# Optimization experiments

Hardware: AMD Instinct MI355X
Metric: run time of the kernel (lower is better)

The kernel has to match this reference:

```python
import jax, jax.numpy as jnp
import numpy as np

H = 1024
V = 50257
S = 2048


def setup_inputs() -> dict:
    key = jax.random.key(0)
    ks = jax.random.split(key, 20)
    sd = 1.0 / np.sqrt(H)
    inp = {
        "input": jax.random.randint(ks[0], (1,), 0, V, dtype=jnp.int64) if jax.config.jax_enable_x64 else jax.random.randint(ks[0], (1,), 0, V, dtype=jnp.int32),
        "hidden": jax.random.normal(ks[1], (1, 1, H), dtype=jnp.float32),
        "encoder_hiddens": jax.random.normal(ks[2], (S, H), dtype=jnp.float32),
        "emb": jax.random.normal(ks[3], (V, H), dtype=jnp.float32),
        "Ua_w": jax.random.normal(ks[4], (H, H), dtype=jnp.float32) * sd,
        "Ua_b": jax.random.normal(ks[5], (H,), dtype=jnp.float32) * sd,
        "Wa_w": jax.random.normal(ks[6], (H, H), dtype=jnp.float32) * sd,
        "Wa_b": jax.random.normal(ks[7], (H,), dtype=jnp.float32) * sd,
        "va": jax.random.normal(ks[8], (1, H), dtype=jnp.float32),
        "comb_w": jax.random.normal(ks[9], (H, 2 * H), dtype=jnp.float32) * sd,
        "comb_b": jax.random.normal(ks[10], (H,), dtype=jnp.float32) * sd,
        "gru_w_ih": jax.random.normal(ks[11], (3 * H, H), dtype=jnp.float32) * sd,
        "gru_w_hh": jax.random.normal(ks[12], (3 * H, H), dtype=jnp.float32) * sd,
        "gru_b_ih": jax.random.normal(ks[13], (3 * H,), dtype=jnp.float32) * sd,
        "gru_b_hh": jax.random.normal(ks[14], (3 * H,), dtype=jnp.float32) * sd,
        "out_w": jax.random.normal(ks[15], (V, 2 * H), dtype=jnp.float32) * sd,
        "out_b": jax.random.normal(ks[16], (V,), dtype=jnp.float32) * sd,
    }
    return inp


def reference(input, hidden, encoder_hiddens, emb, Ua_w, Ua_b, Wa_w, Wa_b, va,
              comb_w, comb_b, gru_w_ih, gru_w_hh, gru_b_ih, gru_b_hh, out_w, out_b):
    # embedded: [1,1,H]  (dropout is identity in eval / p handled at train time)
    embedded = emb[input].reshape(1, 1, H)
    enc = encoder_hiddens[:, None, :]  # [S,1,H]
    # Bahdanau scores: tanh(Ua(enc) + Wa(hidden)) -> [S,1,H]
    scores = jnp.tanh(enc @ Ua_w.T + Ua_b + hidden @ Wa_w.T + Wa_b)
    # torch.inner(va [1,H], scores [S,1,H]) -> [1,S,1]; softmax over S
    attn_weights = jax.nn.softmax(jnp.einsum('oh,sbh->osb', va, scores), axis=1)
    # context: sum_s attn[1,S,1] * enc[S,H] -> [1,H]
    context = jnp.sum(attn_weights * encoder_hiddens, axis=1)
    # combine + relu -> GRU input x: [1,H]
    x = jax.nn.relu(jnp.concatenate([embedded[0], context], axis=1) @ comb_w.T + comb_b)
    # single GRU cell step (PyTorch gate layout: r, z, n)
    h0 = hidden[0]  # [1,H]
    gi = x @ gru_w_ih.T + gru_b_ih
    gh = h0 @ gru_w_hh.T + gru_b_hh
    i_r, i_z, i_n = jnp.split(gi, 3, axis=1)
    h_r, h_z, h_n = jnp.split(gh, 3, axis=1)
    r = jax.nn.sigmoid(i_r + h_r)
    z = jax.nn.sigmoid(i_z + h_z)
    n = jnp.tanh(i_n + r * h_n)
    h_new = (1.0 - z) * n + z * h0  # [1,H]
    hidden_out = h_new[None]  # [1,1,H]
    cat_output = jnp.concatenate([context, h_new], axis=1)  # [1,2H]
    log_probs = jax.nn.log_softmax(cat_output @ out_w.T + out_b, axis=1)  # [1,V]
    return (log_probs, hidden_out, attn_weights)
```

## Files before the change

### kernel.cpp

```cpp
#include <hip/hip_runtime.h>
#include <math.h>

#define H 1024
#define V 50257
#define S 2048

typedef unsigned short u16;
typedef __attribute__((ext_vector_type(8))) short short8;
typedef __attribute__((ext_vector_type(4))) float floatx4;

__device__ __forceinline__ float b2f(u16 b) {
    union { unsigned int u; float f; } x; x.u = ((unsigned int)b) << 16; return x.f;
}
__device__ __forceinline__ u16 f2b(float f) {
    union { float f; unsigned int u; } x; x.f = f;
    unsigned int r = x.u + 0x7FFFu + ((x.u >> 16) & 1u);
    return (u16)(r >> 16);
}

__global__ void __launch_bounds__(256) matvec_kernel(
    const float* __restrict__ W,
    const float* __restrict__ xa, const int* __restrict__ xa_idx, int Ka,
    const float* __restrict__ xb, int Kb,
    const float* __restrict__ bias1,
    float* __restrict__ out, int rows, int relu_flag)
{
    int wave = threadIdx.x >> 6;
    int lane = threadIdx.x & 63;
    int r = blockIdx.x * 4 + wave;
    if (r >= rows) return;
    const float* Wr = W + (size_t)r * (Ka + Kb);
    if (xa_idx) xa += (size_t)(*xa_idx) * Ka;
    float dot = 0.f;
    for (int base = 0; base < Ka; base += 256) {
        int k = base + lane * 4;
        float4 w4 = *reinterpret_cast<const float4*>(Wr + k);
        float4 a4 = *reinterpret_cast<const float4*>(xa + k);
        dot += w4.x * a4.x + w4.y * a4.y + w4.z * a4.z + w4.w * a4.w;
    }
    for (int base = 0; base < Kb; base += 256) {
        int k = base + lane * 4;
        float4 w4 = *reinterpret_cast<const float4*>(Wr + Ka + k);
        float4 a4 = *reinterpret_cast<const float4*>(xb + k);
        dot += w4.x * a4.x + w4.y * a4.y + w4.z * a4.z + w4.w * a4.w;
    }
    #pragma unroll
    for (int off = 32; off; off >>= 1) dot += __shfl_down(dot, off);
    if (lane == 0) {
        float v = dot + bias1[r];
        if (relu_flag) v = fmaxf(v, 0.f);
        out[r] = v;
    }
}

__global__ void __launch_bounds__(256) prep_kernel(
    const float* __restrict__ Wa_w, const float* __restrict__ hidden,
    const float* __restrict__ Wa_b, const float* __restrict__ Ua_b,
    float* __restrict__ u_vec, float* __restrict__ ws_zero,
    const float* __restrict__ enc, const float* __restrict__ Ua,
    u16* __restrict__ enc_hi, u16* __restrict__ enc_lo,
    u16* __restrict__ Ua_hi, u16* __restrict__ Ua_lo)
{
    unsigned int zidx = blockIdx.x * 256 + threadIdx.x;
    if (zidx < 4097) ws_zero[zidx] = 0.f;

    if (blockIdx.x < 256) {
        int wave = threadIdx.x >> 6, lane = threadIdx.x & 63;
        int r = blockIdx.x * 4 + wave;
        const float* Wr = Wa_w + (size_t)r * H;
        float dot = 0.f;
        #pragma unroll
        for (int t = 0; t < 4; t++) {
            int k = t * 256 + lane * 4;
            float4 w4 = *reinterpret_cast<const float4*>(Wr + k);
            float4 a4 = *reinterpret_cast<const float4*>(hidden + k);
            dot += w4.x * a4.x + w4.y * a4.y + w4.z * a4.z + w4.w * a4.w;
        }
        #pragma unroll
        for (int off = 32; off; off >>= 1) dot += __shfl_down(dot, off);
        if (lane == 0) u_vec[r] = dot + Wa_b[r] + Ua_b[r];
        return;
    }
    int idx = (blockIdx.x - 256) * 1024 + threadIdx.x * 4;
    const float* src; u16 *dhi, *dlo; int off;
    if (idx < S * H) { src = enc; dhi = enc_hi; dlo = enc_lo; off = idx; }
    else             { src = Ua;  dhi = Ua_hi;  dlo = Ua_lo;  off = idx - S * H; }
    float4 a = *reinterpret_cast<const float4*>(src + off);
    float av[4] = {a.x, a.y, a.z, a.w};
    ushort4 hi4, lo4;
    u16 hv[4], lv[4];
    #pragma unroll
    for (int i = 0; i < 4; i++) {
        u16 h = f2b(av[i]);
        hv[i] = h;
        lv[i] = f2b(av[i] - b2f(h));
    }
    hi4.x = hv[0]; hi4.y = hv[1]; hi4.z = hv[2]; hi4.w = hv[3];
    lo4.x = lv[0]; lo4.y = lv[1]; lo4.z = lv[2]; lo4.w = lv[3];
    *reinterpret_cast<ushort4*>(dhi + off) = hi4;
    *reinterpret_cast<ushort4*>(dlo + off) = lo4;
}

__global__ void __launch_bounds__(256) attn_scores_kernel(
    const u16* __restrict__ enc_hi, const u16* __restrict__ enc_lo,
    const u16* __restrict__ Ua_hi, const u16* __restrict__ Ua_lo,
    const float* __restrict__ va, const float* __restrict__ u,
    float* __restrict__ attn_logits)
{
    int sgrp  = blockIdx.x & 15;
    int jtile = blockIdx.x >> 4;
    int wave = threadIdx.x >> 6;
    int lane = threadIdx.x & 63;
    int l15 = lane & 15, quad = lane >> 4;
    int s0 = sgrp * 128 + wave * 32, j0 = jtile * 64;

    floatx4 zero4 = {0.f, 0.f, 0.f, 0.f};
    floatx4 acc[2][4];
    #pragma unroll
    for (int ra = 0; ra < 2; ra++)
        #pragma unroll
        for (int cb = 0; cb < 4; cb++) acc[ra][cb] = zero4;

    size_t aoff = (size_t)(s0 + l15) * H + quad * 8;
    size_t boff = (size_t)(j0 + l15) * H + quad * 8;

    for (int k0 = 0; k0 < H; k0 += 32) {
        short8 ah0 = *reinterpret_cast<const short8*>(enc_hi + aoff + k0);
        short8 al0 = *reinterpret_cast<const short8*>(enc_lo + aoff + k0);
        short8 ah1 = *reinterpret_cast<const short8*>(enc_hi + aoff + 16 * H + k0);
        short8 al1 = *reinterpret_cast<const short8*>(enc_lo + aoff + 16 * H + k0);
        #pragma unroll
        for (int cb = 0; cb < 4; cb++) {
            size_t bo = boff + (size_t)cb * 16 * H + k0;
            short8 bh = *reinterpret_cast<const short8*>(Ua_hi + bo);
            short8 bl = *reinterpret_cast<const short8*>(Ua_lo + bo);
            acc[0][cb] = __builtin_amdgcn_mfma_f32_16x16x32_bf16(ah0, bh, acc[0][cb], 0, 0, 0);
            acc[0][cb] = __builtin_amdgcn_mfma_f32_16x16x32_bf16(ah0, bl, acc[0][cb], 0, 0, 0);
            acc[0][cb] = __builtin_amdgcn_mfma_f32_16x16x32_bf16(al0, bh, acc[0][cb], 0, 0, 0);
            acc[1][cb] = __builtin_amdgcn_mfma_f32_16x16x32_bf16(ah1, bh, acc[1][cb], 0, 0, 0);
            acc[1][cb] = __builtin_amdgcn_mfma_f32_16x16x32_bf16(ah1, bl, acc[1][cb], 0, 0, 0);
            acc[1][cb] = __builtin_amdgcn_mfma_f32_16x16x32_bf16(al1, bh, acc[1][cb], 0, 0, 0);
        }
    }

    #pragma unroll
    for (int ra = 0; ra < 2; ra++) {
        #pragma unroll
        for (int reg = 0; reg < 4; reg++) {
            float p = 0.f;
            #pragma unroll
            for (int cb = 0; cb < 4; cb++) {
                int jj = j0 + cb * 16 + l15;
                p += va[jj] * tanhf(acc[ra][cb][reg] + u[jj]);
            }
            p += __shfl_xor(p, 1); p += __shfl_xor(p, 2);
            p += __shfl_xor(p, 4); p += __shfl_xor(p, 8);
            if (l15 == 0)
                atomicAdd(&attn_logits[s0 + ra * 16 + quad * 4 + reg], p);
        }
    }
}

__global__ void __launch_bounds__(256) softmax_context_kernel(
    const float* __restrict__ logits, const float* __restrict__ enc,
    float* __restrict__ ctx, float* __restrict__ attn_out)
{
    __shared__ float red[256];
    __shared__ float sw[16];
    int tid = threadIdx.x;
    float vals[8];
    float m = -1e30f;
    #pragma unroll
    for (int i = 0; i < 8; i++) { vals[i] = logits[tid + 256 * i]; m = fmaxf(m, vals[i]); }
    red[tid] = m; __syncthreads();
    for (int s = 128; s > 0; s >>= 1) {
        if (tid < s) red[tid] = fmaxf(red[tid], red[tid + s]);
        __syncthreads();
    }
    float gmax = red[0]; __syncthreads();
    float sum = 0.f;
    #pragma unroll
    for (int i = 0; i < 8; i++) { vals[i] = expf(vals[i] - gmax); sum += vals[i]; }
    red[tid] = sum; __syncthreads();
    for (int s = 128; s > 0; s >>= 1) {
        if (tid < s) red[tid] += red[tid + s];
        __syncthreads();
    }
    float inv = 1.f / red[0];

    if (blockIdx.x == 0) {
        #pragma unroll
        for (int i = 0; i < 8; i++) attn_out[tid + 256 * i] = vals[i] * inv;
    }

    int sbase = blockIdx.x * 16;
    if (tid < 16) sw[tid] = expf(logits[sbase + tid] - gmax) * inv;
    __syncthreads();

    int h = tid * 4;
    float p0 = 0.f, p1 = 0.f, p2 = 0.f, p3 = 0.f;
    #pragma unroll
    for (int i = 0; i < 16; i++) {
        float w = sw[i];
        float4 e = *reinterpret_cast<const float4*>(enc + (size_t)(sbase + i) * H + h);
        p0 = fmaf(w, e.x, p0); p1 = fmaf(w, e.y, p1);
        p2 = fmaf(w, e.z, p2); p3 = fmaf(w, e.w, p3);
    }
    atomicAdd(&ctx[h + 0], p0); atomicAdd(&ctx[h + 1], p1);
    atomicAdd(&ctx[h + 2], p2); atomicAdd(&ctx[h + 3], p3);
}

__global__ void __launch_bounds__(256) gru_fused_kernel(
    const float* __restrict__ w_ih, const float* __restrict__ w_hh,
    const float* __restrict__ x, const float* __restrict__ h0,
    const float* __restrict__ b_ih, const float* __restrict__ b_hh,
    float* __restrict__ cat_hnew, float* __restrict__ out_hidden)
{
    int wave = threadIdx.x >> 6, lane = threadIdx.x & 63;
    int j = blockIdx.x * 4 + wave;
    float d[6] = {0.f, 0.f, 0.f, 0.f, 0.f, 0.f};
    #pragma unroll
    for (int t = 0; t < 4; t++) {
        int k = t * 256 + lane * 4;
        float4 xv = *reinterpret_cast<const float4*>(x + k);
        float4 hv = *reinterpret_cast<const float4*>(h0 + k);
        #pragma unroll
        for (int g = 0; g < 3; g++) {
            float4 wi = *reinterpret_cast<const float4*>(w_ih + (size_t)(g * H + j) * H + k);
            float4 wh = *reinterpret_cast<const float4*>(w_hh + (size_t)(g * H + j) * H + k);
            d[g]     += wi.x * xv.x + wi.y * xv.y + wi.z * xv.z + wi.w * xv.w;
            d[3 + g] += wh.x * hv.x + wh.y * hv.y + wh.z * hv.z + wh.w * hv.w;
        }
    }
    #pragma unroll
    for (int off = 32; off; off >>= 1)
        #pragma unroll
        for (int g = 0; g < 6; g++) d[g] += __shfl_down(d[g], off);
    if (lane == 0) {
        float i_r = d[0] + b_ih[j];
        float i_z = d[1] + b_ih[H + j];
        float i_n = d[2] + b_ih[2 * H + j];
        float h_r = d[3] + b_hh[j];
        float h_z = d[4] + b_hh[H + j];
        float h_n = d[5] + b_hh[2 * H + j];
        float r = 1.f / (1.f + expf(-(i_r + h_r)));
        float z = 1.f / (1.f + expf(-(i_z + h_z)));
        float n = tanhf(i_n + r * h_n);
        float hn = (1.f - z) * n + z * h0[j];
        cat_hnew[j] = hn;
        out_hidden[j] = hn;
    }
}

__global__ void __launch_bounds__(256) out_matvec_kernel(
    const float* __restrict__ Wout, const float* __restrict__ bout,
    const float* __restrict__ cat, float* __restrict__ logits,
    float* __restrict__ separtial)
{
    __shared__ float cs[2 * H];
    __shared__ float wred[4];
    for (int i = threadIdx.x; i < 2 * H; i += 256) cs[i] = cat[i];
    __syncthreads();
    int wave = threadIdx.x >> 6, lane = threadIdx.x & 63;
    float lsum = 0.f;
    for (int v = blockIdx.x * 4 + wave; v < V; v += gridDim.x * 4) {
        const float* Wr = Wout + (size_t)v * (2 * H);
        float dot = 0.f;
        #pragma unroll
        for (int t = 0; t < 8; t++) {
            int k = t * 256 + lane * 4;
            float4 w4 = *reinterpret_cast<const float4*>(Wr + k);
            dot += w4.x * cs[k] + w4.y * cs[k + 1] + w4.z * cs[k + 2] + w4.w * cs[k + 3];
        }
        #pragma unroll
        for (int off = 32; off; off >>= 1) dot += __shfl_down(dot, off);
        if (lane == 0) {
            dot += bout[v];
            logits[v] = dot;
            lsum += expf(dot);
        }
    }
    if (lane == 0) wred[wave] = lsum;
    __syncthreads();
    if (threadIdx.x == 0)
        separtial[blockIdx.x] = wred[0] + wred[1] + wred[2] + wred[3];
}

__global__ void __launch_bounds__(256) logsoftmax_kernel(
    float* __restrict__ logits, const float* __restrict__ separtial)
{
    __shared__ float red[256];
    int tid = threadIdx.x;
    float s = 0.f;
    #pragma unroll
    for (int i = 0; i < 8; i++) s += separtial[tid + 256 * i];
    red[tid] = s; __syncthreads();
    for (int st = 128; st > 0; st >>= 1) {
        if (tid < st) red[tid] += red[tid + st];
        __syncthreads();
    }
    float lz = logf(red[0]);
    int v = blockIdx.x * 256 + tid;
    if (v < V) logits[v] -= lz;
}

extern "C" void kernel_launch(void* const* d_in, const int* in_sizes, int n_in,
                              void* d_out, int out_size, void* d_ws, size_t ws_size,
                              hipStream_t stream)
{
    const int*   token  = (const int*)d_in[0];
    const float* hidden = (const float*)d_in[1];
    const float* enc    = (const float*)d_in[2];
    const float* emb    = (const float*)d_in[3];
    const float* Ua_w   = (const float*)d_in[4];
    const float* Ua_b   = (const float*)d_in[5];
    const float* Wa_w   = (const float*)d_in[6];
    const float* Wa_b   = (const float*)d_in[7];
    const float* va     = (const float*)d_in[8];
    const float* comb_w = (const float*)d_in[9];
    const float* comb_b = (const float*)d_in[10];
    const float* w_ih   = (const float*)d_in[11];
    const float* w_hh   = (const float*)d_in[12];
    const float* b_ih   = (const float*)d_in[13];
    const float* b_hh   = (const float*)d_in[14];
    const float* out_w  = (const float*)d_in[15];
    const float* out_b  = (const float*)d_in[16];
    float* out = (float*)d_out;

    float* ws          = (float*)d_ws;
    float* attn_logits = ws + 0;
    float* cat         = ws + 2048;
    float* u_vec       = ws + 4608;
    float* x_vec       = ws + 5632;
    float* separtial   = ws + 6656;

    char* wsb   = (char*)d_ws;
    u16* enc_hi = (u16*)(wsb + 65536);
    u16* enc_lo = (u16*)(wsb + 65536 + 4u * 1024 * 1024);
    u16* Ua_hi  = (u16*)(wsb + 65536 + 8u * 1024 * 1024);
    u16* Ua_lo  = (u16*)(wsb + 65536 + 10u * 1024 * 1024);

    prep_kernel<<<3328, 256, 0, stream>>>(Wa_w, hidden, Wa_b, Ua_b, u_vec, ws,
                                          enc, Ua_w, enc_hi, enc_lo, Ua_hi, Ua_lo);
    attn_scores_kernel<<<256, 256, 0, stream>>>(enc_hi, enc_lo, Ua_hi, Ua_lo,
                                                va, u_vec, attn_logits);
    softmax_context_kernel<<<128, 256, 0, stream>>>(attn_logits, enc, cat,
                                                    out + V + H);
    matvec_kernel<<<256, 256, 0, stream>>>(comb_w, emb, token, H, cat, H,
                                           comb_b, x_vec, H, 1);
    gru_fused_kernel<<<256, 256, 0, stream>>>(w_ih, w_hh, x_vec, hidden,
                                              b_ih, b_hh, cat + H, out + V);
    out_matvec_kernel<<<2048, 256, 0, stream>>>(out_w, out_b, cat, out, separtial);
    logsoftmax_kernel<<<(V + 255) / 256, 256, 0, stream>>>(out, separtial);
}
```

Measured before the change: 751.2 us.

## Fuse attention, softmax-context, combine and GRU into one persistent kernel with grid barriers

Merges the attention-score MFMA, softmax+context, combine matvec and GRU input matvec into a single 256-block kernel separated by atomic spin grid barriers, removing three kernel launches and their gaps. The hidden-state GRU matvec (w_hh·h) is moved into the prep kernel as extra blocks since it depends only on inputs. The context reduction now uses 256 blocks of 8 rows instead of 128 of 16. This relies on all blocks being co-resident for the barrier to avoid deadlock, and adds spin-wait overhead.

Result: slower. 807.0 us (+7.4%).

```diff
diff --git a/kernel.cpp b/kernel.cpp
--- a/kernel.cpp
+++ b/kernel.cpp
@@ -4,6 +4,7 @@
 #define H 1024
 #define V 50257
 #define S 2048
+#define NBLK 256
 
 typedef unsigned short u16;
 typedef __attribute__((ext_vector_type(8))) short short8;
@@ -18,39 +19,17 @@
     return (u16)(r >> 16);
 }
 
-__global__ void __launch_bounds__(256) matvec_kernel(
-    const float* __restrict__ W,
-    const float* __restrict__ xa, const int* __restrict__ xa_idx, int Ka,
-    const float* __restrict__ xb, int Kb,
-    const float* __restrict__ bias1,
-    float* __restrict__ out, int rows, int relu_flag)
-{
-    int wave = threadIdx.x >> 6;
-    int lane = threadIdx.x & 63;
-    int r = blockIdx.x * 4 + wave;
-    if (r >= rows) return;
-    const float* Wr = W + (size_t)r * (Ka + Kb);
-    if (xa_idx) xa += (size_t)(*xa_idx) * Ka;
-    float dot = 0.f;
-    for (int base = 0; base < Ka; base += 256) {
-        int k = base + lane * 4;
-        float4 w4 = *reinterpret_cast<const float4*>(Wr + k);
-        float4 a4 = *reinterpret_cast<const float4*>(xa + k);
-        dot += w4.x * a4.x + w4.y * a4.y + w4.z * a4.z + w4.w * a4.w;
-    }
-    for (int base = 0; base < Kb; base += 256) {
-        int k = base + lane * 4;
-        float4 w4 = *reinterpret_cast<const float4*>(Wr + Ka + k);
-        float4 a4 = *reinterpret_cast<const float4*>(xb + k);
-        dot += w4.x * a4.x + w4.y * a4.y + w4.z * a4.z + w4.w * a4.w;
-    }
-    #pragma unroll
-    for (int off = 32; off; off >>= 1) dot += __shfl_down(dot, off);
-    if (lane == 0) {
-        float v = dot + bias1[r];
-        if (relu_flag) v = fmaxf(v, 0.f);
-        out[r] = v;
-    }
+__device__ __forceinline__ void grid_barrier(int* cnt) {
+    __syncthreads();
+    if (threadIdx.x == 0) {
+        __threadfence();
+        __hip_atomic_fetch_add(cnt, 1, __ATOMIC_ACQ_REL, __HIP_MEMORY_SCOPE_AGENT);
+        while (__hip_atomic_load(cnt, __ATOMIC_ACQUIRE, __HIP_MEMORY_SCOPE_AGENT) < NBLK) {
+            __builtin_amdgcn_s_sleep(1);
+        }
+        __threadfence();
+    }
+    __syncthreads();
 }
 
 __global__ void __launch_bounds__(256) prep_kernel(
@@ -59,10 +38,11 @@
     float* __restrict__ u_vec, float* __restrict__ ws_zero,
     const float* __restrict__ enc, const float* __restrict__ Ua,
     u16* __restrict__ enc_hi, u16* __restrict__ enc_lo,
-    u16* __restrict__ Ua_hi, u16* __restrict__ Ua_lo)
+    u16* __restrict__ Ua_hi, u16* __restrict__ Ua_lo,
+    const float* __restrict__ w_hh, float* __restrict__ gh)
 {
     unsigned int zidx = blockIdx.x * 256 + threadIdx.x;
-    if (zidx < 4097) ws_zero[zidx] = 0.f;
+    if (zidx < 4104) ws_zero[zidx] = 0.f;
 
     if (blockIdx.x < 256) {
         int wave = threadIdx.x >> 6, lane = threadIdx.x & 63;
@@ -81,174 +61,233 @@
         if (lane == 0) u_vec[r] = dot + Wa_b[r] + Ua_b[r];
         return;
     }
-    int idx = (blockIdx.x - 256) * 1024 + threadIdx.x * 4;
-    const float* src; u16 *dhi, *dlo; int off;
-    if (idx < S * H) { src = enc; dhi = enc_hi; dlo = enc_lo; off = idx; }
-    else             { src = Ua;  dhi = Ua_hi;  dlo = Ua_lo;  off = idx - S * H; }
-    float4 a = *reinterpret_cast<const float4*>(src + off);
-    float av[4] = {a.x, a.y, a.z, a.w};
-    ushort4 hi4, lo4;
-    u16 hv[4], lv[4];
-    #pragma unroll
-    for (int i = 0; i < 4; i++) {
-        u16 h = f2b(av[i]);
-        hv[i] = h;
-        lv[i] = f2b(av[i] - b2f(h));
-    }
-    hi4.x = hv[0]; hi4.y = hv[1]; hi4.z = hv[2]; hi4.w = hv[3];
-    lo4.x = lv[0]; lo4.y = lv[1]; lo4.z = lv[2]; lo4.w = lv[3];
-    *reinterpret_cast<ushort4*>(dhi + off) = hi4;
-    *reinterpret_cast<ushort4*>(dlo + off) = lo4;
-}
-
-__global__ void __launch_bounds__(256) attn_scores_kernel(
+    if (blockIdx.x < 3328) {
+        int idx = (blockIdx.x - 256) * 1024 + threadIdx.x * 4;
+        const float* src; u16 *dhi, *dlo; int off;
+        if (idx < S * H) { src = enc; dhi = enc_hi; dlo = enc_lo; off = idx; }
+        else             { src = Ua;  dhi = Ua_hi;  dlo = Ua_lo;  off = idx - S * H; }
+        float4 a = *reinterpret_cast<const float4*>(src + off);
+        float av[4] = {a.x, a.y, a.z, a.w};
+        ushort4 hi4, lo4;
+        u16 hv[4], lv[4];
+        #pragma unroll
+        for (int i = 0; i < 4; i++) {
+            u16 h = f2b(av[i]);
+            hv[i] = h;
+            lv[i] = f2b(av[i] - b2f(h));
+        }
+        hi4.x = hv[0]; hi4.y = hv[1]; hi4.z = hv[2]; hi4.w = hv[3];
+        lo4.x = lv[0]; lo4.y = lv[1]; lo4.z = lv[2]; lo4.w = lv[3];
+        *reinterpret_cast<ushort4*>(dhi + off) = hi4;
+        *reinterpret_cast<ushort4*>(dlo + off) = lo4;
+        return;
+    }
+    {
+        int wave = threadIdx.x >> 6, lane = threadIdx.x & 63;
+        int j = (blockIdx.x - 3328) * 4 + wave;
+        float d0 = 0.f, d1 = 0.f, d2 = 0.f;
+        #pragma unroll
+        for (int t = 0; t < 4; t++) {
+            int k = t * 256 + lane * 4;
+            float4 hv = *reinterpret_cast<const float4*>(hidden + k);
+            float4 w0 = *reinterpret_cast<const float4*>(w_hh + (size_t)(0 * H + j) * H + k);
+            float4 w1 = *reinterpret_cast<const float4*>(w_hh + (size_t)(1 * H + j) * H + k);
+            float4 w2 = *reinterpret_cast<const float4*>(w_hh + (size_t)(2 * H + j) * H + k);
+            d0 += w0.x * hv.x + w0.y * hv.y + w0.z * hv.z + w0.w * hv.w;
+            d1 += w1.x * hv.x + w1.y * hv.y + w1.z * hv.z + w1.w * hv.w;
+            d2 += w2.x * hv.x + w2.y * hv.y + w2.z * hv.z + w2.w * hv.w;
+        }
+        #pragma unroll
+        for (int off = 32; off; off >>= 1) {
+            d0 += __shfl_down(d0, off);
+            d1 += __shfl_down(d1, off);
+            d2 += __shfl_down(d2, off);
+        }
+        if (lane == 0) { gh[j] = d0; gh[H + j] = d1; gh[2 * H + j] = d2; }
+    }
+}
+
+__global__ void __launch_bounds__(256) mega_kernel(
     const u16* __restrict__ enc_hi, const u16* __restrict__ enc_lo,
     const u16* __restrict__ Ua_hi, const u16* __restrict__ Ua_lo,
     const float* __restrict__ va, const float* __restrict__ u,
-    float* __restrict__ attn_logits)
-{
-    int sgrp  = blockIdx.x & 15;
-    int jtile = blockIdx.x >> 4;
-    int wave = threadIdx.x >> 6;
-    int lane = threadIdx.x & 63;
-    int l15 = lane & 15, quad = lane >> 4;
-    int s0 = sgrp * 128 + wave * 32, j0 = jtile * 64;
-
-    floatx4 zero4 = {0.f, 0.f, 0.f, 0.f};
-    floatx4 acc[2][4];
-    #pragma unroll
-    for (int ra = 0; ra < 2; ra++)
-        #pragma unroll
-        for (int cb = 0; cb < 4; cb++) acc[ra][cb] = zero4;
-
-    size_t aoff = (size_t)(s0 + l15) * H + quad * 8;
-    size_t boff = (size_t)(j0 + l15) * H + quad * 8;
-
-    for (int k0 = 0; k0 < H; k0 += 32) {
-        short8 ah0 = *reinterpret_cast<const short8*>(enc_hi + aoff + k0);
-        short8 al0 = *reinterpret_cast<const short8*>(enc_lo + aoff + k0);
-        short8 ah1 = *reinterpret_cast<const short8*>(enc_hi + aoff + 16 * H + k0);
-        short8 al1 = *reinterpret_cast<const short8*>(enc_lo + aoff + 16 * H + k0);
-        #pragma unroll
-        for (int cb = 0; cb < 4; cb++) {
-            size_t bo = boff + (size_t)cb * 16 * H + k0;
-            short8 bh = *reinterpret_cast<const short8*>(Ua_hi + bo);
-            short8 bl = *reinterpret_cast<const short8*>(Ua_lo + bo);
-            acc[0][cb] = __builtin_amdgcn_mfma_f32_16x16x32_bf16(ah0, bh, acc[0][cb], 0, 0, 0);
-            acc[0][cb] = __builtin_amdgcn_mfma_f32_16x16x32_bf16(ah0, bl, acc[0][cb], 0, 0, 0);
-            acc[0][cb] = __builtin_amdgcn_mfma_f32_16x16x32_bf16(al0, bh, acc[0][cb], 0, 0, 0);
-            acc[1][cb] = __builtin_amdgcn_mfma_f32_16x16x32_bf16(ah1, bh, acc[1][cb], 0, 0, 0);
-            acc[1][cb] = __builtin_amdgcn_mfma_f32_16x16x32_bf16(ah1, bl, acc[1][cb], 0, 0, 0);
-            acc[1][cb] = __builtin_amdgcn_mfma_f32_16x16x32_bf16(al1, bh, acc[1][cb], 0, 0, 0);
-        }
-    }
-
-    #pragma unroll
-    for (int ra = 0; ra < 2; ra++) {
-        #pragma unroll
-        for (int reg = 0; reg < 4; reg++) {
-            float p = 0.f;
+    float* __restrict__ attn_logits,
+    const float* __restrict__ enc, float* __restrict__ cat,
+    float* __restrict__ attn_out,
+    const float* __restrict__ comb_w, const float* __restrict__ comb_b,
+    const float* __restrict__ emb, const int* __restrict__ token,
+    float* __restrict__ x_vec,
+    const float* __restrict__ w_ih, const float* __restrict__ b_ih,
+    const float* __restrict__ b_hh, const float* __restrict__ gh,
+    const float* __restrict__ hidden, float* __restrict__ out_hidden,
+    int* __restrict__ bars)
+{
+    __shared__ float red[256];
+    __shared__ float sw[8];
+    int tid  = threadIdx.x;
+    int wave = tid >> 6;
+    int lane = tid & 63;
+
+    {
+        int sgrp  = blockIdx.x & 15;
+        int jtile = blockIdx.x >> 4;
+        int l15 = lane & 15, quad = lane >> 4;
+        int s0 = sgrp * 128 + wave * 32, j0 = jtile * 64;
+
+        floatx4 zero4 = {0.f, 0.f, 0.f, 0.f};
+        floatx4 acc[2][4];
+        #pragma unroll
+        for (int ra = 0; ra < 2; ra++)
+            #pragma unroll
+            for (int cb = 0; cb < 4; cb++) acc[ra][cb] = zero4;
+
+        size_t aoff = (size_t)(s0 + l15) * H + quad * 8;
+        size_t boff = (size_t)(j0 + l15) * H + quad * 8;
+
+        for (int k0 = 0; k0 < H; k0 += 32) {
+            short8 ah0 = *reinterpret_cast<const short8*>(enc_hi + aoff + k0);
+            short8 al0 = *reinterpret_cast<const short8*>(enc_lo + aoff + k0);
+            short8 ah1 = *reinterpret_cast<const short8*>(enc_hi + aoff + 16 * H + k0);
+            short8 al1 = *reinterpret_cast<const short8*>(enc_lo + aoff + 16 * H + k0);
             #pragma unroll
             for (int cb = 0; cb < 4; cb++) {
-                int jj = j0 + cb * 16 + l15;
-                p += va[jj] * tanhf(acc[ra][cb][reg] + u[jj]);
+                size_t bo = boff + (size_t)cb * 16 * H + k0;
+                short8 bh = *reinterpret_cast<const short8*>(Ua_hi + bo);
+                short8 bl = *reinterpret_cast<const short8*>(Ua_lo + bo);
+                acc[0][cb] = __builtin_amdgcn_mfma_f32_16x16x32_bf16(ah0, bh, acc[0][cb], 0, 0, 0);
+                acc[0][cb] = __builtin_amdgcn_mfma_f32_16x16x32_bf16(ah0, bl, acc[0][cb], 0, 0, 0);
+                acc[0][cb] = __builtin_amdgcn_mfma_f32_16x16x32_bf16(al0, bh, acc[0][cb], 0, 0, 0);
+                acc[1][cb] = __builtin_amdgcn_mfma_f32_16x16x32_bf16(ah1, bh, acc[1][cb], 0, 0, 0);
+                acc[1][cb] = __builtin_amdgcn_mfma_f32_16x16x32_bf16(ah1, bl, acc[1][cb], 0, 0, 0);
+                acc[1][cb] = __builtin_amdgcn_mfma_f32_16x16x32_bf16(al1, bh, acc[1][cb], 0, 0, 0);
             }
-            p += __shfl_xor(p, 1); p += __shfl_xor(p, 2);
-            p += __shfl_xor(p, 4); p += __shfl_xor(p, 8);
-            if (l15 == 0)
-                atomicAdd(&attn_logits[s0 + ra * 16 + quad * 4 + reg], p);
-        }
-    }
-}
-
-__global__ void __launch_bounds__(256) softmax_context_kernel(
-    const float* __restrict__ logits, const float* __restrict__ enc,
-    float* __restrict__ ctx, float* __restrict__ attn_out)
-{
-    __shared__ float red[256];
-    __shared__ float sw[16];
-    int tid = threadIdx.x;
-    float vals[8];
-    float m = -1e30f;
-    #pragma unroll
-    for (int i = 0; i < 8; i++) { vals[i] = logits[tid + 256 * i]; m = fmaxf(m, vals[i]); }
-    red[tid] = m; __syncthreads();
-    for (int s = 128; s > 0; s >>= 1) {
-        if (tid < s) red[tid] = fmaxf(red[tid], red[tid + s]);
+        }
+
+        #pragma unroll
+        for (int ra = 0; ra < 2; ra++) {
+            #pragma unroll
+            for (int reg = 0; reg < 4; reg++) {
+                float p = 0.f;
+                #pragma unroll
+                for (int cb = 0; cb < 4; cb++) {
+                    int jj = j0 + cb * 16 + l15;
+                    p += va[jj] * tanhf(acc[ra][cb][reg] + u[jj]);
+                }
+                p += __shfl_xor(p, 1); p += __shfl_xor(p, 2);
+                p += __shfl_xor(p, 4); p += __shfl_xor(p, 8);
+                if (l15 == 0)
+                    atomicAdd(&attn_logits[s0 + ra * 16 + quad * 4 + reg], p);
+            }
+        }
+    }
+
+    grid_barrier(bars + 0);
+
+    {
+        float vals[8];
+        float m = -1e30f;
+        #pragma unroll
+        for (int i = 0; i < 8; i++) { vals[i] = attn_logits[tid + 256 * i]; m = fmaxf(m, vals[i]); }
+        red[tid] = m; __syncthreads();
+        for (int s = 128; s > 0; s >>= 1) {
+            if (tid < s) red[tid] = fmaxf(red[tid], red[tid + s]);
+            __syncthreads();
+        }
+        float gmax = red[0]; __syncthreads();
+        float sum = 0.f;
+        #pragma unroll
+        for (int i = 0; i < 8; i++) { vals[i] = expf(vals[i] - gmax); sum += vals[i]; }
+        red[tid] = sum; __syncthreads();
+        for (int s = 128; s > 0; s >>= 1) {
+            if (tid < s) red[tid] += red[tid + s];
+            __syncthreads();
+        }
+        float inv = 1.f / red[0];
+
+        if (blockIdx.x == 0) {
+            #pragma unroll
+            for (int i = 0; i < 8; i++) attn_out[tid + 256 * i] = vals[i] * inv;
+        }
+
+        int sbase = blockIdx.x * 8;
+        if (tid < 8) sw[tid] = expf(attn_logits[sbase + tid] - gmax) * inv;
         __syncthreads();
-    }
-    float gmax = red[0]; __syncthreads();
-    float sum = 0.f;
-    #pragma unroll
-    for (int i = 0; i < 8; i++) { vals[i] = expf(vals[i] - gmax); sum += vals[i]; }
-    red[tid] = sum; __syncthreads();
-    for (int s = 128; s > 0; s >>= 1) {
-        if (tid < s) red[tid] += red[tid + s];
-        __syncthreads();
-    }
-    float inv = 1.f / red[0];
-
-    if (blockIdx.x == 0) {
-        #pragma unroll
-        for (int i = 0; i < 8; i++) attn_out[tid + 256 * i] = vals[i] * inv;
-    }
-
-    int sbase = blockIdx.x * 16;
-    if (tid < 16) sw[tid] = expf(logits[sbase + tid] - gmax) * inv;
-    __syncthreads();
-
-    int h = tid * 4;
-    float p0 = 0.f, p1 = 0.f, p2 = 0.f, p3 = 0.f;
-    #pragma unroll
-    for (int i = 0; i < 16; i++) {
-        float w = sw[i];
-        float4 e = *reinterpret_cast<const float4*>(enc + (size_t)(sbase + i) * H + h);
-        p0 = fmaf(w, e.x, p0); p1 = fmaf(w, e.y, p1);
-        p2 = fmaf(w, e.z, p2); p3 = fmaf(w, e.w, p3);
-    }
-    atomicAdd(&ctx[h + 0], p0); atomicAdd(&ctx[h + 1], p1);
-    atomicAdd(&ctx[h + 2], p2); atomicAdd(&ctx[h + 3], p3);
-}
-
-__global__ void __launch_bounds__(256) gru_fused_kernel(
-    const float* __restrict__ w_ih, const float* __restrict__ w_hh,
-    const float* __restrict__ x, const float* __restrict__ h0,
-    const float* __restrict__ b_ih, const float* __restrict__ b_hh,
-    float* __restrict__ cat_hnew, float* __restrict__ out_hidden)
-{
-    int wave = threadIdx.x >> 6, lane = threadIdx.x & 63;
-    int j = blockIdx.x * 4 + wave;
-    float d[6] = {0.f, 0.f, 0.f, 0.f, 0.f, 0.f};
-    #pragma unroll
-    for (int t = 0; t < 4; t++) {
-        int k = t * 256 + lane * 4;
-        float4 xv = *reinterpret_cast<const float4*>(x + k);
-        float4 hv = *reinterpret_cast<const float4*>(h0 + k);
-        #pragma unroll
-        for (int g = 0; g < 3; g++) {
-            float4 wi = *reinterpret_cast<const float4*>(w_ih + (size_t)(g * H + j) * H + k);
-            float4 wh = *reinterpret_cast<const float4*>(w_hh + (size_t)(g * H + j) * H + k);
-            d[g]     += wi.x * xv.x + wi.y * xv.y + wi.z * xv.z + wi.w * xv.w;
-            d[3 + g] += wh.x * hv.x + wh.y * hv.y + wh.z * hv.z + wh.w * hv.w;
-        }
-    }
-    #pragma unroll
-    for (int off = 32; off; off >>= 1)
-        #pragma unroll
-        for (int g = 0; g < 6; g++) d[g] += __shfl_down(d[g], off);
-    if (lane == 0) {
-        float i_r = d[0] + b_ih[j];
-        float i_z = d[1] + b_ih[H + j];
-        float i_n = d[2] + b_ih[2 * H + j];
-        float h_r = d[3] + b_hh[j];
-        float h_z = d[4] + b_hh[H + j];
-        float h_n = d[5] + b_hh[2 * H + j];
-        float r = 1.f / (1.f + expf(-(i_r + h_r)));
-        float z = 1.f / (1.f + expf(-(i_z + h_z)));
-        float n = tanhf(i_n + r * h_n);
-        float hn = (1.f - z) * n + z * h0[j];
-        cat_hnew[j] = hn;
-        out_hidden[j] = hn;
+
+        int h = tid * 4;
+        float p0 = 0.f, p1 = 0.f, p2 = 0.f, p3 = 0.f;
+        #pragma unroll
+        for (int i = 0; i < 8; i++) {
+            float w = sw[i];
+            float4 e = *reinterpret_cast<const float4*>(enc + (size_t)(sbase + i) * H + h);
+            p0 = fmaf(w, e.x, p0); p1 = fmaf(w, e.y, p1);
+            p2 = fmaf(w, e.z, p2); p3 = fmaf(w, e.w, p3);
+        }
+        atomicAdd(&cat[h + 0], p0); atomicAdd(&cat[h + 1], p1);
+        atomicAdd(&cat[h + 2], p2); atomicAdd(&cat[h + 3], p3);
+    }
+
+    grid_barrier(bars + 1);
+
+    {
+        int r = blockIdx.x * 4 + wave;
+        const float* Wr = comb_w + (size_t)r * (2 * H);
+        const float* erow = emb + (size_t)(*token) * H;
+        float dot = 0.f;
+        #pragma unroll
+        for (int t = 0; t < 4; t++) {
+            int k = t * 256 + lane * 4;
+            float4 w4 = *reinterpret_cast<const float4*>(Wr + k);
+            float4 a4 = *reinterpret_cast<const float4*>(erow + k);
+            dot += w4.x * a4.x + w4.y * a4.y + w4.z * a4.z + w4.w * a4.w;
+        }
+        #pragma unroll
+        for (int t = 0; t < 4; t++) {
+            int k = t * 256 + lane * 4;
+            float4 w4 = *reinterpret_cast<const float4*>(Wr + H + k);
+            float4 a4 = *reinterpret_cast<const float4*>(cat + k);
+            dot += w4.x * a4.x + w4.y * a4.y + w4.z * a4.z + w4.w * a4.w;
+        }
+        #pragma unroll
+        for (int off = 32; off; off >>= 1) dot += __shfl_down(dot, off);
+        if (lane == 0) x_vec[r] = fmaxf(dot + comb_b[r], 0.f);
+    }
+
+    grid_barrier(bars + 2);
+
+    {
+        int j = blockIdx.x * 4 + wave;
+        float d0 = 0.f, d1 = 0.f, d2 = 0.f;
+        #pragma unroll
+        for (int t = 0; t < 4; t++) {
+            int k = t * 256 + lane * 4;
+            float4 xv = *reinterpret_cast<const float4*>(x_vec + k);
+            float4 w0 = *reinterpret_cast<const float4*>(w_ih + (size_t)(0 * H + j) * H + k);
+            float4 w1 = *reinterpret_cast<const float4*>(w_ih + (size_t)(1 * H + j) * H + k);
+            float4 w2 = *reinterpret_cast<const float4*>(w_ih + (size_t)(2 * H + j) * H + k);
+            d0 += w0.x * xv.x + w0.y * xv.y + w0.z * xv.z + w0.w * xv.w;
+            d1 += w1.x * xv.x + w1.y * xv.y + w1.z * xv.z + w1.w * xv.w;
+            d2 += w2.x * xv.x + w2.y * xv.y + w2.z * xv.z + w2.w * xv.w;
+        }
+        #pragma unroll
+        for (int off = 32; off; off >>= 1) {
+            d0 += __shfl_down(d0, off);
+            d1 += __shfl_down(d1, off);
+            d2 += __shfl_down(d2, off);
+        }
+        if (lane == 0) {
+            float i_r = d0 + b_ih[j];
+            float i_z = d1 + b_ih[H + j];
+            float i_n = d2 + b_ih[2 * H + j];
+            float h_r = gh[j] + b_hh[j];
+            float h_z = gh[H + j] + b_hh[H + j];
+            float h_n = gh[2 * H + j] + b_hh[2 * H + j];
+            float r = 1.f / (1.f + expf(-(i_r + h_r)));
+            float z = 1.f / (1.f + expf(-(i_z + h_z)));
+            float n = tanhf(i_n + r * h_n);
+            float hn = (1.f - z) * n + z * hidden[j];
+            cat[H + j] = hn;
+            out_hidden[j] = hn;
+        }
     }
 }
 
@@ -330,9 +369,11 @@
     float* ws          = (float*)d_ws;
     float* attn_logits = ws + 0;
     float* cat         = ws + 2048;
+    int*   bars        = (int*)(ws + 4100);
     float* u_vec       = ws + 4608;
     float* x_vec       = ws + 5632;
     float* separtial   = ws + 6656;
+    float* gh          = ws + 8704;
 
     char* wsb   = (char*)d_ws;
     u16* enc_hi = (u16*)(wsb + 65536);
@@ -340,16 +381,15 @@
     u16* Ua_hi  = (u16*)(wsb + 65536 + 8u * 1024 * 1024);
     u16* Ua_lo  = (u16*)(wsb + 65536 + 10u * 1024 * 1024);
 
-    prep_kernel<<<3328, 256, 0, stream>>>(Wa_w, hidden, Wa_b, Ua_b, u_vec, ws,
-                                          enc, Ua_w, enc_hi, enc_lo, Ua_hi, Ua_lo);
-    attn_scores_kernel<<<256, 256, 0, stream>>>(enc_hi, enc_lo, Ua_hi, Ua_lo,
-                                                va, u_vec, attn_logits);
-    softmax_context_kernel<<<128, 256, 0, stream>>>(attn_logits, enc, cat,
-                                                    out + V + H);
-    matvec_kernel<<<256, 256, 0, stream>>>(comb_w, emb, token, H, cat, H,
-                                           comb_b, x_vec, H, 1);
-    gru_fused_kernel<<<256, 256, 0, stream>>>(w_ih, w_hh, x_vec, hidden,
-                                              b_ih, b_hh, cat + H, out + V);
+    prep_kernel<<<3584, 256, 0, stream>>>(Wa_w, hidden, Wa_b, Ua_b, u_vec, ws,
+                                          enc, Ua_w, enc_hi, enc_lo, Ua_hi, Ua_lo,
+                                          w_hh, gh);
+    mega_kernel<<<NBLK, 256, 0, stream>>>(enc_hi, enc_lo, Ua_hi, Ua_lo,
+                                          va, u_vec, attn_logits,
+                                          enc, cat, out + V + H,
+                                          comb_w, comb_b, emb, token, x_vec,
+                                          w_ih, b_ih, b_hh, gh, hidden,
+                                          out + V, bars);
     out_matvec_kernel<<<2048, 256, 0, stream>>>(out_w, out_b, cat, out, separtial);
     logsoftmax_kernel<<<(V + 255) / 256, 256, 0, stream>>>(out, separtial);
 }
```

## Hoist GRU hidden-side matvec into prep kernel and widen context grid

Applied to the files above, without the earlier changes.

The W_hh·h0 GRU matvec depends only on the input hidden state, so it moves into the early prep kernel as 256 extra blocks. The GRU kernel on the critical path then streams only W_ih. The softmax/context kernel also doubles its grid to 256 blocks of 8 rows each, which raises parallelism at the cost of more atomic adds on ctx. The zeroing range grows slightly and gh gets its own workspace slot.

New measurement: 763.3 us. Within noise of the previous version (+1.6%).

```diff
diff --git a/kernel.cpp b/kernel.cpp
--- a/kernel.cpp
+++ b/kernel.cpp
@@ -59,10 +59,11 @@
     float* __restrict__ u_vec, float* __restrict__ ws_zero,
     const float* __restrict__ enc, const float* __restrict__ Ua,
     u16* __restrict__ enc_hi, u16* __restrict__ enc_lo,
-    u16* __restrict__ Ua_hi, u16* __restrict__ Ua_lo)
+    u16* __restrict__ Ua_hi, u16* __restrict__ Ua_lo,
+    const float* __restrict__ w_hh, float* __restrict__ gh)
 {
     unsigned int zidx = blockIdx.x * 256 + threadIdx.x;
-    if (zidx < 4097) ws_zero[zidx] = 0.f;
+    if (zidx < 4104) ws_zero[zidx] = 0.f;
 
     if (blockIdx.x < 256) {
         int wave = threadIdx.x >> 6, lane = threadIdx.x & 63;
@@ -81,24 +82,50 @@
         if (lane == 0) u_vec[r] = dot + Wa_b[r] + Ua_b[r];
         return;
     }
-    int idx = (blockIdx.x - 256) * 1024 + threadIdx.x * 4;
-    const float* src; u16 *dhi, *dlo; int off;
-    if (idx < S * H) { src = enc; dhi = enc_hi; dlo = enc_lo; off = idx; }
-    else             { src = Ua;  dhi = Ua_hi;  dlo = Ua_lo;  off = idx - S * H; }
-    float4 a = *reinterpret_cast<const float4*>(src + off);
-    float av[4] = {a.x, a.y, a.z, a.w};
-    ushort4 hi4, lo4;
-    u16 hv[4], lv[4];
-    #pragma unroll
-    for (int i = 0; i < 4; i++) {
-        u16 h = f2b(av[i]);
-        hv[i] = h;
-        lv[i] = f2b(av[i] - b2f(h));
-    }
-    hi4.x = hv[0]; hi4.y = hv[1]; hi4.z = hv[2]; hi4.w = hv[3];
-    lo4.x = lv[0]; lo4.y = lv[1]; lo4.z = lv[2]; lo4.w = lv[3];
-    *reinterpret_cast<ushort4*>(dhi + off) = hi4;
-    *reinterpret_cast<ushort4*>(dlo + off) = lo4;
+    if (blockIdx.x < 3328) {
+        int idx = (blockIdx.x - 256) * 1024 + threadIdx.x * 4;
+        const float* src; u16 *dhi, *dlo; int off;
+        if (idx < S * H) { src = enc; dhi = enc_hi; dlo = enc_lo; off = idx; }
+        else             { src = Ua;  dhi = Ua_hi;  dlo = Ua_lo;  off = idx - S * H; }
+        float4 a = *reinterpret_cast<const float4*>(src + off);
+        float av[4] = {a.x, a.y, a.z, a.w};
+        ushort4 hi4, lo4;
+        u16 hv[4], lv[4];
+        #pragma unroll
+        for (int i = 0; i < 4; i++) {
+            u16 h = f2b(av[i]);
+            hv[i] = h;
+            lv[i] = f2b(av[i] - b2f(h));
+        }
+        hi4.x = hv[0]; hi4.y = hv[1]; hi4.z = hv[2]; hi4.w = hv[3];
+        lo4.x = lv[0]; lo4.y = lv[1]; lo4.z = lv[2]; lo4.w = lv[3];
+        *reinterpret_cast<ushort4*>(dhi + off) = hi4;
+        *reinterpret_cast<ushort4*>(dlo + off) = lo4;
+        return;
+    }
+    {
+        int wave = threadIdx.x >> 6, lane = threadIdx.x & 63;
+        int j = (blockIdx.x - 3328) * 4 + wave;
+        float d0 = 0.f, d1 = 0.f, d2 = 0.f;
+        #pragma unroll
+        for (int t = 0; t < 4; t++) {
+            int k = t * 256 + lane * 4;
+            float4 hv = *reinterpret_cast<const float4*>(hidden + k);
+            float4 w0 = *reinterpret_cast<const float4*>(w_hh + (size_t)(0 * H + j) * H + k);
+            float4 w1 = *reinterpret_cast<const float4*>(w_hh + (size_t)(1 * H + j) * H + k);
+            float4 w2 = *reinterpret_cast<const float4*>(w_hh + (size_t)(2 * H + j) * H + k);
+            d0 += w0.x * hv.x + w0.y * hv.y + w0.z * hv.z + w0.w * hv.w;
+            d1 += w1.x * hv.x + w1.y * hv.y + w1.z * hv.z + w1.w * hv.w;
+            d2 += w2.x * hv.x + w2.y * hv.y + w2.z * hv.z + w2.w * hv.w;
+        }
+        #pragma unroll
+        for (int off = 32; off; off >>= 1) {
+            d0 += __shfl_down(d0, off);
+            d1 += __shfl_down(d1, off);
+            d2 += __shfl_down(d2, off);
+        }
+        if (lane == 0) { gh[j] = d0; gh[H + j] = d1; gh[2 * H + j] = d2; }
+    }
 }
 
 __global__ void __launch_bounds__(256) attn_scores_kernel(
@@ -166,7 +193,7 @@
     float* __restrict__ ctx, float* __restrict__ attn_out)
 {
     __shared__ float red[256];
-    __shared__ float sw[16];
+    __shared__ float sw[8];
     int tid = threadIdx.x;
     float vals[8];
     float m = -1e30f;
@@ -193,14 +220,14 @@
         for (int i = 0; i < 8; i++) attn_out[tid + 256 * i] = vals[i] * inv;
     }
 
-    int sbase = blockIdx.x * 16;
-    if (tid < 16) sw[tid] = expf(logits[sbase + tid] - gmax) * inv;
+    int sbase = blockIdx.x * 8;
+    if (tid < 8) sw[tid] = expf(logits[sbase + tid] - gmax) * inv;
     __syncthreads();
 
     int h = tid * 4;
     float p0 = 0.f, p1 = 0.f, p2 = 0.f, p3 = 0.f;
     #pragma unroll
-    for (int i = 0; i < 16; i++) {
+    for (int i = 0; i < 8; i++) {
         float w = sw[i];
         float4 e = *reinterpret_cast<const float4*>(enc + (size_t)(sbase + i) * H + h);
         p0 = fmaf(w, e.x, p0); p1 = fmaf(w, e.y, p1);
@@ -210,39 +237,39 @@
     atomicAdd(&ctx[h + 2], p2); atomicAdd(&ctx[h + 3], p3);
 }
 
-__global__ void __launch_bounds__(256) gru_fused_kernel(
-    const float* __restrict__ w_ih, const float* __restrict__ w_hh,
-    const float* __restrict__ x, const float* __restrict__ h0,
-    const float* __restrict__ b_ih, const float* __restrict__ b_hh,
+__global__ void __launch_bounds__(256) gru_x_kernel(
+    const float* __restrict__ w_ih, const float* __restrict__ x,
+    const float* __restrict__ gh, const float* __restrict__ b_ih,
+    const float* __restrict__ b_hh, const float* __restrict__ h0,
     float* __restrict__ cat_hnew, float* __restrict__ out_hidden)
 {
     int wave = threadIdx.x >> 6, lane = threadIdx.x & 63;
     int j = blockIdx.x * 4 + wave;
-    float d[6] = {0.f, 0.f, 0.f, 0.f, 0.f, 0.f};
+    float d0 = 0.f, d1 = 0.f, d2 = 0.f;
     #pragma unroll
     for (int t = 0; t < 4; t++) {
         int k = t * 256 + lane * 4;
         float4 xv = *reinterpret_cast<const float4*>(x + k);
-        float4 hv = *reinterpret_cast<const float4*>(h0 + k);
-        #pragma unroll
-        for (int g = 0; g < 3; g++) {
-            float4 wi = *reinterpret_cast<const float4*>(w_ih + (size_t)(g * H + j) * H + k);
-            float4 wh = *reinterpret_cast<const float4*>(w_hh + (size_t)(g * H + j) * H + k);
-            d[g]     += wi.x * xv.x + wi.y * xv.y + wi.z * xv.z + wi.w * xv.w;
-            d[3 + g] += wh.x * hv.x + wh.y * hv.y + wh.z * hv.z + wh.w * hv.w;
-        }
-    }
-    #pragma unroll
-    for (int off = 32; off; off >>= 1)
-        #pragma unroll
-        for (int g = 0; g < 6; g++) d[g] += __shfl_down(d[g], off);
+        float4 w0 = *reinterpret_cast<const float4*>(w_ih + (size_t)(0 * H + j) * H + k);
+        float4 w1 = *reinterpret_cast<const float4*>(w_ih + (size_t)(1 * H + j) * H + k);
+        float4 w2 = *reinterpret_cast<const float4*>(w_ih + (size_t)(2 * H + j) * H + k);
+        d0 += w0.x * xv.x + w0.y * xv.y + w0.z * xv.z + w0.w * xv.w;
+        d1 += w1.x * xv.x + w1.y * xv.y + w1.z * xv.z + w1.w * xv.w;
+        d2 += w2.x * xv.x + w2.y * xv.y + w2.z * xv.z + w2.w * xv.w;
+    }
+    #pragma unroll
+    for (int off = 32; off; off >>= 1) {
+        d0 += __shfl_down(d0, off);
+        d1 += __shfl_down(d1, off);
+        d2 += __shfl_down(d2, off);
+    }
     if (lane == 0) {
-        float i_r = d[0] + b_ih[j];
-        float i_z = d[1] + b_ih[H + j];
-        float i_n = d[2] + b_ih[2 * H + j];
-        float h_r = d[3] + b_hh[j];
-        float h_z = d[4] + b_hh[H + j];
-        float h_n = d[5] + b_hh[2 * H + j];
+        float i_r = d0 + b_ih[j];
+        float i_z = d1 + b_ih[H + j];
+        float i_n = d2 + b_ih[2 * H + j];
+        float h_r = gh[j] + b_hh[j];
+        float h_z = gh[H + j] + b_hh[H + j];
+        float h_n = gh[2 * H + j] + b_hh[2 * H + j];
         float r = 1.f / (1.f + expf(-(i_r + h_r)));
         float z = 1.f / (1.f + expf(-(i_z + h_z)));
         float n = tanhf(i_n + r * h_n);
@@ -333,6 +360,7 @@
     float* u_vec       = ws + 4608;
     float* x_vec       = ws + 5632;
     float* separtial   = ws + 6656;
+    float* gh          = ws + 8704;
 
     char* wsb   = (char*)d_ws;
     u16* enc_hi = (u16*)(wsb + 65536);
@@ -340,16 +368,17 @@
     u16* Ua_hi  = (u16*)(wsb + 65536 + 8u * 1024 * 1024);
     u16* Ua_lo  = (u16*)(wsb + 65536 + 10u * 1024 * 1024);
 
-    prep_kernel<<<3328, 256, 0, stream>>>(Wa_w, hidden, Wa_b, Ua_b, u_vec, ws,
-                                          enc, Ua_w, enc_hi, enc_lo, Ua_hi, Ua_lo);
+    prep_kernel<<<3584, 256, 0, stream>>>(Wa_w, hidden, Wa_b, Ua_b, u_vec, ws,
+                                          enc, Ua_w, enc_hi, enc_lo, Ua_hi, Ua_lo,
+                                          w_hh, gh);
     attn_scores_kernel<<<256, 256, 0, stream>>>(enc_hi, enc_lo, Ua_hi, Ua_lo,
                                                 va, u_vec, attn_logits);
-    softmax_context_kernel<<<128, 256, 0, stream>>>(attn_logits, enc, cat,
+    softmax_context_kernel<<<256, 256, 0, stream>>>(attn_logits, enc, cat,
                                                     out + V + H);
     matvec_kernel<<<256, 256, 0, stream>>>(comb_w, emb, token, H, cat, H,
                                            comb_b, x_vec, H, 1);
-    gru_fused_kernel<<<256, 256, 0, stream>>>(w_ih, w_hh, x_vec, hidden,
-                                              b_ih, b_hh, cat + H, out + V);
+    gru_x_kernel<<<256, 256, 0, stream>>>(w_ih, x_vec, gh, b_ih, b_hh, hidden,
+                                          cat + H, out + V);
     out_matvec_kernel<<<2048, 256, 0, stream>>>(out_w, out_b, cat, out, separtial);
     logsoftmax_kernel<<<(V + 255) / 256, 256, 0, stream>>>(out, separtial);
 }
```
